# Performance work log

Measured on AMD Instinct MI355X. Metric: run time of the kernel, lower is better.

Reference implementation:

```python
import jax, jax.numpy as jnp
import numpy as np
from jax import lax

NUM_HEADS = 8
EPS = 1e-12  # F.normalize default eps


def _l2norm(t):
    # F.normalize(t, dim=-1): t / max(||t||_2, eps)
    n = jnp.sqrt(jnp.sum(t * t, axis=-1, keepdims=True))
    return t / jnp.maximum(n, EPS)


def setup_inputs() -> dict:
    key = jax.random.key(0)
    k1, k2, k3, k4 = jax.random.split(key, 4)
    b, c, h, w = 16, 384, 64, 64
    x = jax.random.normal(k1, (b, c, h, w), dtype=jnp.float32)
    # 1x1 conv weights stored as (out, in); depthwise 3x3 as (3c, 1, 3, 3)
    w_qkv = jax.random.normal(k2, (3 * c, c), dtype=jnp.float32) * (1.0 / np.sqrt(c))
    w_dw = jax.random.normal(k3, (3 * c, 1, 3, 3), dtype=jnp.float32) * (1.0 / 3.0)
    w_proj = jax.random.normal(k4, (c, c), dtype=jnp.float32) * (1.0 / np.sqrt(c))
    temperature = jnp.ones((1, NUM_HEADS, 1, 1), dtype=jnp.float32)
    return {"x": x, "w_qkv": w_qkv, "w_dw": w_dw, "w_proj": w_proj,
            "temperature": temperature}


def reference(x, w_qkv, w_dw, w_proj, temperature):
    b, c, h, w = x.shape
    hw = h * w
    d = c // NUM_HEADS  # per-head channel dim

    # 1x1 pointwise conv: (b,c,h,w) x (3c,c) -> (b,3c,h,w)
    qkv = jnp.einsum('bchw,oc->bohw', x, w_qkv)
    # depthwise 3x3 conv, groups = 3c, padding SAME, no bias
    qkv = lax.conv_general_dilated(
        qkv, w_dw, window_strides=(1, 1), padding='SAME',
        feature_group_count=3 * c,
        dimension_numbers=('NCHW', 'OIHW', 'NCHW'))

    q, k, v = jnp.split(qkv, 3, axis=1)
    q = q.reshape(b, NUM_HEADS, d, hw)
    k = k.reshape(b, NUM_HEADS, d, hw)
    v = v.reshape(b, NUM_HEADS, d, hw)

    q = _l2norm(q)
    k = _l2norm(k)

    # transposed (channel) attention: scores over channel dim, (b,H,d,d)
    scores = jnp.einsum('bhdn,bhen->bhde', q, k) * temperature
    attn = jax.nn.softmax(scores, axis=-1)

    out = jnp.einsum('bhde,bhen->bhdn', attn, v).reshape(b, c, h, w)
    out = jnp.einsum('bchw,oc->bohw', out, w_proj)
    return out
```

## Files before the change

kernel.cpp:

```cpp
#include <hip/hip_runtime.h>
#include <hip/hip_bf16.h>
#include <math.h>

#define B_   16
#define C_   384
#define C3_  1152
#define HW_  4096
#define NH_  8
#define D_   48

typedef _Float16 f16x8 __attribute__((ext_vector_type(8)));
typedef _Float16 f16x4 __attribute__((ext_vector_type(4)));
typedef _Float16 f16x2 __attribute__((ext_vector_type(2)));
typedef float    f32x4 __attribute__((ext_vector_type(4)));

#define ASM_VMCNT(n) asm volatile("s_waitcnt vmcnt(" #n ")" ::: "memory")

__global__ __launch_bounds__(256) void conv_w_all(
    const float* __restrict__ wqkv, const float* __restrict__ wproj,
    _Float16* __restrict__ oq, _Float16* __restrict__ op)
{
    const int nq = C3_ * C_ / 4;
    const int np = C_ * C_ / 4;
    int i = blockIdx.x * 256 + threadIdx.x;
    const float* src; _Float16* dst; int j;
    if (i < nq) { src = wqkv; dst = oq; j = i; }
    else if (i < nq + np) { src = wproj; dst = op; j = i - nq; }
    else return;
    float4 v = *(const float4*)&src[(size_t)j * 4];
    f16x4 h = { (_Float16)v.x, (_Float16)v.y, (_Float16)v.z, (_Float16)v.w };
    *(f16x4*)&dst[(size_t)j * 4] = h;
}

__global__ __launch_bounds__(256) void transpose_to_f16(
    const float* __restrict__ x, _Float16* __restrict__ xt)
{
    const int b  = blockIdx.z;
    const int k0 = blockIdx.y * 64;
    const int n0 = blockIdx.x * 64;
    __shared__ float sm[64][65];
    const float* xb = x + (size_t)b * C_ * HW_;
    _Float16* xtb = xt + (size_t)b * HW_ * C_;
    const int t = threadIdx.x;
    #pragma unroll
    for (int i = 0; i < 4; ++i) {
        int row = (t >> 4) + i * 16;
        int col = (t & 15) * 4;
        float4 v = *(const float4*)&xb[(size_t)(k0 + row) * HW_ + n0 + col];
        sm[row][col] = v.x; sm[row][col+1] = v.y; sm[row][col+2] = v.z; sm[row][col+3] = v.w;
    }
    __syncthreads();
    #pragma unroll
    for (int i = 0; i < 2; ++i) {
        int nl = (t >> 3) + i * 32;
        int ks = (t & 7) * 8;
        f16x8 h;
        #pragma unroll
        for (int j = 0; j < 8; ++j) h[j] = (_Float16)sm[ks + j][nl];
        *(f16x8*)&xtb[(size_t)(n0 + nl) * C_ + k0 + ks] = h;
    }
}

template<int M, bool F32OUT>
__global__ __launch_bounds__(256, 2) void mfma_gemm(
    const _Float16* __restrict__ Wb,
    const _Float16* __restrict__ XT,
    void* __restrict__ Cv, long long xstride, long long cstride)
{
    constexpr int K = 384;
    constexpr int BK = 32;
    constexpr int NSTEP = K / BK;
    constexpr int MB = M / 128;
    __shared__ _Float16 LDS[36864];
    _Float16* Ash = LDS;
    _Float16* Bsh = LDS + 3 * 128 * BK;

    const int nwg = MB * 16 * B_;
    const int cpx = nwg >> 3;
    const int bid = blockIdx.x;
    const int L   = (bid & 7) * cpx + (bid >> 3);
    const int m0  = (L % MB) * 128;
    const int nb  = L / MB;
    const int n0  = (nb & 15) * 256;
    const int b   = nb >> 4;

    const _Float16* __restrict__ XTb = XT + (size_t)b * xstride;
    const int t = threadIdx.x;
    const int l = t & 63, w = t >> 6;
    const int frow = l & 15, kseg16 = l >> 4;

    auto stage = [&](int d, int kt) {
        const int kk = kt * BK;
        #pragma unroll
        for (int i = 0; i < 2; ++i) {
            const int u = i * 256 + t;
            const int row = u >> 2, slot = u & 3;
            const int scol = slot ^ (row & 3) ^ ((row >> 2) & 1);
            const _Float16* ga = Wb + (size_t)(m0 + row) * K + kk + scol * 8;
            __builtin_amdgcn_global_load_lds(
                (const __attribute__((address_space(1))) void*)ga,
                (__attribute__((address_space(3))) void*)((char*)(Ash + d * 128 * BK) + u * 16),
                16, 0, 0);
        }
        #pragma unroll
        for (int i = 0; i < 4; ++i) {
            const int u = i * 256 + t;
            const int row = u >> 2, slot = u & 3;
            const int scol = slot ^ (row & 3) ^ ((row >> 2) & 1);
            const _Float16* gb = XTb + (size_t)(n0 + row) * K + kk + scol * 8;
            __builtin_amdgcn_global_load_lds(
                (const __attribute__((address_space(1))) void*)gb,
                (__attribute__((address_space(3))) void*)((char*)(Bsh + d * 256 * BK) + u * 16),
                16, 0, 0);
        }
    };

    f32x4 acc[8][4] = {};

    stage(0, 0); stage(1, 1);
    #pragma unroll
    for (int kt = 0; kt < NSTEP; ++kt) {
        const int cur = kt % 3;
        if (kt + 1 < NSTEP) { ASM_VMCNT(6); } else { ASM_VMCNT(0); }
        __builtin_amdgcn_sched_barrier(0);
        __builtin_amdgcn_s_barrier();
        __builtin_amdgcn_sched_barrier(0);
        if (kt + 2 < NSTEP) stage((kt + 2) % 3, kt + 2);
        f16x8 af[8], bfr[4];
        #pragma unroll
        for (int mi = 0; mi < 8; ++mi) {
            const int rA = mi * 16 + frow;
            const int cs = kseg16 ^ (rA & 3) ^ ((rA >> 2) & 1);
            af[mi] = *(const f16x8*)&Ash[cur * 128 * BK + rA * BK + cs * 8];
        }
        #pragma unroll
        for (int ni = 0; ni < 4; ++ni) {
            const int rB = w * 64 + ni * 16 + frow;
            const int cs = kseg16 ^ (rB & 3) ^ ((rB >> 2) & 1);
            bfr[ni] = *(const f16x8*)&Bsh[cur * 256 * BK + rB * BK + cs * 8];
        }
        __builtin_amdgcn_s_setprio(1);
        #pragma unroll
        for (int mi = 0; mi < 8; ++mi)
            #pragma unroll
            for (int ni = 0; ni < 4; ++ni)
                acc[mi][ni] = __builtin_amdgcn_mfma_f32_16x16x32_f16(
                    bfr[ni], af[mi], acc[mi][ni], 0, 0, 0);
        __builtin_amdgcn_s_setprio(0);
    }

    __syncthreads();
    char* tbase = (char*)LDS + w * 17408;
    if constexpr (!F32OUT) {
        #pragma unroll
        for (int mi = 0; mi < 8; ++mi)
            #pragma unroll
            for (int ni = 0; ni < 4; ++ni) {
                const int row = mi * 16 + (l & 15);
                const int pxl = ni * 16 + (l >> 4) * 4;
                f16x2 lo = { (_Float16)acc[mi][ni][0], (_Float16)acc[mi][ni][1] };
                f16x2 hi = { (_Float16)acc[mi][ni][2], (_Float16)acc[mi][ni][3] };
                *(f16x2*)(tbase + row * 136 + pxl * 2)     = lo;
                *(f16x2*)(tbase + row * 136 + pxl * 2 + 4) = hi;
            }
        asm volatile("s_waitcnt lgkmcnt(0)" ::: "memory");
        __builtin_amdgcn_sched_barrier(0);
        _Float16* Co = (_Float16*)Cv + (size_t)b * cstride;
        #pragma unroll
        for (int j = 0; j < 16; ++j) {
            const int ch = j * 8 + (l >> 3);
            const int px = (l & 7) * 8;
            f16x4 lo = *(const f16x4*)(tbase + ch * 136 + px * 2);
            f16x4 hi = *(const f16x4*)(tbase + ch * 136 + px * 2 + 8);
            f16x8 v;
            #pragma unroll
            for (int q = 0; q < 4; ++q) { v[q] = lo[q]; v[q + 4] = hi[q]; }
            *(f16x8*)&Co[(size_t)(m0 + ch) * HW_ + n0 + w * 64 + px] = v;
        }
    } else {
        float* Co = (float*)Cv + (size_t)b * cstride;
        #pragma unroll
        for (int p = 0; p < 2; ++p) {
            if (p) { asm volatile("s_waitcnt lgkmcnt(0)" ::: "memory");
                     __builtin_amdgcn_sched_barrier(0); }
            #pragma unroll
            for (int mi = 0; mi < 4; ++mi)
                #pragma unroll
                for (int ni = 0; ni < 4; ++ni) {
                    const int row = mi * 16 + (l & 15);
                    const int pxl = ni * 16 + (l >> 4) * 4;
                    float2 lo = make_float2(acc[p * 4 + mi][ni][0], acc[p * 4 + mi][ni][1]);
                    float2 hi = make_float2(acc[p * 4 + mi][ni][2], acc[p * 4 + mi][ni][3]);
                    *(float2*)(tbase + row * 272 + pxl * 4)     = lo;
                    *(float2*)(tbase + row * 272 + pxl * 4 + 8) = hi;
                }
            asm volatile("s_waitcnt lgkmcnt(0)" ::: "memory");
            __builtin_amdgcn_sched_barrier(0);
            #pragma unroll
            for (int j = 0; j < 16; ++j) {
                const int lch = j * 4 + (l >> 4);
                const int ch  = p * 64 + lch;
                const int px  = (l & 15) * 4;
                float2 lo = *(const float2*)(tbase + lch * 272 + px * 4);
                float2 hi = *(const float2*)(tbase + lch * 272 + px * 4 + 8);
                f32x4 v = { lo.x, lo.y, hi.x, hi.y };
                *(f32x4*)&Co[(size_t)(m0 + ch) * HW_ + n0 + w * 64 + px] = v;
            }
        }
    }
}

__global__ __launch_bounds__(256) void dwconv_norm(
    _Float16* __restrict__ buf, const float* __restrict__ wdw,
    float* __restrict__ nqinv, float* __restrict__ nkinv)
{
    const int plane = blockIdx.x;
    const int ch = plane % C3_, b = plane / C3_;
    __shared__ _Float16 smh[64 * 72];
    __shared__ float wsum[4];
    _Float16* g = buf + (size_t)plane * HW_;
    const int t = threadIdx.x;
    #pragma unroll
    for (int i = 0; i < 2; ++i) {
        const int u = i * 256 + t;
        f16x8 v = *(const f16x8*)&g[u * 8];
        *(f16x8*)&smh[(u >> 3) * 72 + (u & 7) * 8] = v;
    }
    float w[9];
    #pragma unroll
    for (int j = 0; j < 9; ++j) w[j] = wdw[ch * 9 + j];
    __syncthreads();
    float ssq = 0.f;
    #pragma unroll
    for (int i = 0; i < 2; ++i) {
        const int u = i * 256 + t;
        const int y = u >> 3, c0 = (u & 7) * 8;
        float r[3][10];
        #pragma unroll
        for (int dy = 0; dy < 3; ++dy) {
            const int yy = y + dy - 1;
            if (yy < 0 || yy > 63) {
                #pragma unroll
                for (int j = 0; j < 10; ++j) r[dy][j] = 0.f;
            } else {
                f16x8 v = *(const f16x8*)&smh[yy * 72 + c0];
                #pragma unroll
                for (int j = 0; j < 8; ++j) r[dy][j + 1] = (float)v[j];
                r[dy][0] = (c0 > 0)  ? (float)smh[yy * 72 + c0 - 1] : 0.f;
                r[dy][9] = (c0 < 56) ? (float)smh[yy * 72 + c0 + 8] : 0.f;
            }
        }
        f16x8 o;
        #pragma unroll
        for (int j = 0; j < 8; ++j) {
            float s = 0.f;
            #pragma unroll
            for (int dy = 0; dy < 3; ++dy)
                #pragma unroll
                for (int dx = 0; dx < 3; ++dx)
                    s = fmaf(w[dy * 3 + dx], r[dy][j + dx], s);
            o[j] = (_Float16)s;
            ssq = fmaf(s, s, ssq);
        }
        *(f16x8*)&g[u * 8] = o;
    }
    if (ch < 2 * C_) {
        #pragma unroll
        for (int m = 1; m < 64; m <<= 1) ssq += __shfl_xor(ssq, m);
        if ((t & 63) == 0) wsum[t >> 6] = ssq;
        __syncthreads();
        if (t == 0) {
            float tot = wsum[0] + wsum[1] + wsum[2] + wsum[3];
            float inv = 1.f / fmaxf(sqrtf(tot), 1e-12f);
            (ch < C_ ? nqinv : nkinv)[b * C_ + (ch % C_)] = inv;
        }
    }
}

__global__ __launch_bounds__(256) void scores_mfma(
    const _Float16* __restrict__ buf, float* __restrict__ sp)
{
    const int bh = blockIdx.x;
    const int ks = blockIdx.y;
    const int b = bh >> 3, h = bh & 7;
    const _Float16* qbase = buf + ((size_t)b * C3_ + (size_t)h * D_) * HW_;
    const _Float16* kbase = qbase + (size_t)C_ * HW_;
    const int t = threadIdx.x, l = t & 63, w = t >> 6;
    const int frow = l & 15, kseg = (l >> 4) * 8;
    const int p0 = ks * 1024 + w * 256;

    f32x4 acc[3][3] = {};
    #pragma unroll 2
    for (int st = 0; st < 8; ++st) {
        const int p = p0 + st * 32 + kseg;
        f16x8 qf[3], kf[3];
        #pragma unroll
        for (int mi = 0; mi < 3; ++mi)
            qf[mi] = *(const f16x8*)&qbase[(size_t)(mi * 16 + frow) * HW_ + p];
        #pragma unroll
        for (int ni = 0; ni < 3; ++ni)
            kf[ni] = *(const f16x8*)&kbase[(size_t)(ni * 16 + frow) * HW_ + p];
        #pragma unroll
        for (int mi = 0; mi < 3; ++mi)
            #pragma unroll
            for (int ni = 0; ni < 3; ++ni)
                acc[mi][ni] = __builtin_amdgcn_mfma_f32_16x16x32_f16(
                    qf[mi], kf[ni], acc[mi][ni], 0, 0, 0);
    }
    __shared__ float red[4][D_ * D_];
    #pragma unroll
    for (int mi = 0; mi < 3; ++mi)
        #pragma unroll
        for (int ni = 0; ni < 3; ++ni)
            #pragma unroll
            for (int r = 0; r < 4; ++r)
                red[w][(mi * 16 + (l >> 4) * 4 + r) * D_ + ni * 16 + (l & 15)] =
                    acc[mi][ni][r];
    __syncthreads();
    float* out = sp + ((size_t)ks * 128 + bh) * (D_ * D_);
    const float* rf = &red[0][0];
    for (int i = t; i < D_ * D_; i += 256)
        out[i] = rf[i] + rf[2304 + i] + rf[4608 + i] + rf[6912 + i];
}

__global__ __launch_bounds__(256) void softmax_k(
    const float* __restrict__ sp, const float* __restrict__ nqinv,
    const float* __restrict__ nkinv, const float* __restrict__ temp,
    float* __restrict__ attn)
{
    const int row = blockIdx.x * 4 + (threadIdx.x >> 6);
    const int bh = row / D_, d = row % D_;
    const int h = bh & 7;
    const int e = threadIdx.x & 63;
    float s = -INFINITY;
    if (e < D_) {
        float raw = 0.f;
        #pragma unroll
        for (int ks = 0; ks < 4; ++ks)
            raw += sp[((size_t)ks * 128 + bh) * (D_ * D_) + d * D_ + e];
        s = raw * nqinv[bh * D_ + d] * nkinv[bh * D_ + e] * temp[h];
    }
    float m = s;
    #pragma unroll
    for (int off = 1; off < 64; off <<= 1) m = fmaxf(m, __shfl_xor(m, off));
    float p = (e < D_) ? expf(s - m) : 0.f;
    float sum = p;
    #pragma unroll
    for (int off = 1; off < 64; off <<= 1) sum += __shfl_xor(sum, off);
    if (e < D_) attn[(size_t)bh * (D_ * D_) + d * D_ + e] = p / sum;
}

__global__ __launch_bounds__(256) void pv_kernel(
    _Float16* __restrict__ buf, const float* __restrict__ attn)
{
    const int b = blockIdx.z, h = blockIdx.y;
    const int p0 = blockIdx.x * 512 + threadIdx.x * 2;
    __shared__ float a4[48][48];
    const float* ab = attn + ((size_t)b * 8 + h) * (D_ * D_);
    for (int i = threadIdx.x; i < D_ * D_; i += 256) ((float*)a4)[i] = ab[i];
    __syncthreads();
    const _Float16* vbase = buf + ((size_t)b * C3_ + 2 * C_ + (size_t)h * D_) * HW_;
    float2 acc[48];
    #pragma unroll
    for (int d = 0; d < 48; ++d) { acc[d].x = 0.f; acc[d].y = 0.f; }
    #pragma unroll 1
    for (int e4 = 0; e4 < 12; ++e4) {
        float2 vv[4];
        #pragma unroll
        for (int j = 0; j < 4; ++j) {
            f16x2 h2 = *(const f16x2*)&vbase[(size_t)(e4 * 4 + j) * HW_ + p0];
            vv[j].x = (float)h2[0]; vv[j].y = (float)h2[1];
        }
        #pragma unroll
        for (int d = 0; d < 48; ++d) {
            float4 a = *(const float4*)&a4[d][e4 * 4];
            acc[d].x = fmaf(a.x, vv[0].x, fmaf(a.y, vv[1].x, fmaf(a.z, vv[2].x, fmaf(a.w, vv[3].x, acc[d].x))));
            acc[d].y = fmaf(a.x, vv[0].y, fmaf(a.y, vv[1].y, fmaf(a.z, vv[2].y, fmaf(a.w, vv[3].y, acc[d].y))));
        }
    }
    _Float16* xt2b = buf + (size_t)b * C3_ * HW_;
    #pragma unroll
    for (int px = 0; px < 2; ++px) {
        f16x8 tmp[6];
        #pragma unroll
        for (int d = 0; d < 48; ++d) tmp[d >> 3][d & 7] = (_Float16)(px ? acc[d].y : acc[d].x);
        f16x8* dst = (f16x8*)&xt2b[(size_t)(p0 + px) * C_ + h * D_];
        #pragma unroll
        for (int j = 0; j < 6; ++j) dst[j] = tmp[j];
    }
}

extern "C" void kernel_launch(void* const* d_in, const int* in_sizes, int n_in,
                              void* d_out, int out_size, void* d_ws, size_t ws_size,
                              hipStream_t stream)
{
    const float* x      = (const float*)d_in[0];
    const float* w_qkv  = (const float*)d_in[1];
    const float* w_dw   = (const float*)d_in[2];
    const float* w_proj = (const float*)d_in[3];
    const float* temp   = (const float*)d_in[4];
    float* out = (float*)d_out;

    _Float16* buf = (_Float16*)d_ws;
    float* nqinv = (float*)(buf + (size_t)B_ * C3_ * HW_);
    float* nkinv = nqinv + 6144;
    float* sp    = nkinv + 6144;
    float* attn  = sp + (size_t)4 * 128 * D_ * D_;
    _Float16* wqkv_h  = (_Float16*)(attn + (size_t)128 * D_ * D_);
    _Float16* wproj_h = wqkv_h + (size_t)C3_ * C_;
    _Float16* xt1     = wproj_h + (size_t)C_ * C_;

    conv_w_all<<<(C3_ * C_ / 4 + C_ * C_ / 4 + 255) / 256, 256, 0, stream>>>(
        w_qkv, w_proj, wqkv_h, wproj_h);
    transpose_to_f16<<<dim3(64, 6, 16), 256, 0, stream>>>(x, xt1);

    mfma_gemm<C3_, false><<<dim3(9 * 16 * 16), 256, 0, stream>>>(
        wqkv_h, xt1, buf, (long long)HW_ * C_, (long long)C3_ * HW_);

    dwconv_norm<<<B_ * C3_, 256, 0, stream>>>(buf, w_dw, nqinv, nkinv);

    scores_mfma<<<dim3(128, 4), 256, 0, stream>>>(buf, sp);

    softmax_k<<<1536, 256, 0, stream>>>(sp, nqinv, nkinv, temp, attn);

    pv_kernel<<<dim3(8, 8, 16), 256, 0, stream>>>(buf, attn);

    mfma_gemm<C_, true><<<dim3(3 * 16 * 16), 256, 0, stream>>>(
        wproj_h, buf, out, (long long)C3_ * HW_, (long long)C_ * HW_);
}
```

Measured before the change: 268.4 us.

## Use 8-wave GEMM blocks with 4-stage LDS ring and double-buffered fragments

The MFMA GEMM now runs 512 threads per block as a 2x4 wave grid, so each wave holds a 64x64 accumulator tile instead of 128x64. The global-to-LDS pipeline grows from 3 to 4 stages, and register fragments are double-buffered so the LDS reads for step k+1 overlap the MFMAs for step k. The aim is to cut per-wave register pressure and hide LDS and global latency better. In exchange, occupancy drops to one block per CU, LDS use grows, and each wave does less work per LDS fragment load.

Measured after the change: 287.7 us. +7.2%, slower.

```diff
diff --git a/kernel.cpp b/kernel.cpp
--- a/kernel.cpp
+++ b/kernel.cpp
@@ -62,7 +62,7 @@
 }
 
 template<int M, bool F32OUT>
-__global__ __launch_bounds__(256, 2) void mfma_gemm(
+__global__ __launch_bounds__(512, 1) void mfma_gemm(
     const _Float16* __restrict__ Wb,
     const _Float16* __restrict__ XT,
     void* __restrict__ Cv, long long xstride, long long cstride)
@@ -71,9 +71,7 @@
     constexpr int BK = 32;
     constexpr int NSTEP = K / BK;
     constexpr int MB = M / 128;
-    __shared__ _Float16 LDS[36864];
-    _Float16* Ash = LDS;
-    _Float16* Bsh = LDS + 3 * 128 * BK;
+    __shared__ _Float16 LDS[49152];
 
     const int nwg = MB * 16 * B_;
     const int cpx = nwg >> 3;
@@ -87,73 +85,84 @@
     const _Float16* __restrict__ XTb = XT + (size_t)b * xstride;
     const int t = threadIdx.x;
     const int l = t & 63, w = t >> 6;
+    const int wm = w >> 2, wn = w & 3;
     const int frow = l & 15, kseg16 = l >> 4;
 
     auto stage = [&](int d, int kt) {
         const int kk = kt * BK;
-        #pragma unroll
-        for (int i = 0; i < 2; ++i) {
-            const int u = i * 256 + t;
-            const int row = u >> 2, slot = u & 3;
+        {
+            const int row = t >> 2, slot = t & 3;
             const int scol = slot ^ (row & 3) ^ ((row >> 2) & 1);
             const _Float16* ga = Wb + (size_t)(m0 + row) * K + kk + scol * 8;
             __builtin_amdgcn_global_load_lds(
                 (const __attribute__((address_space(1))) void*)ga,
-                (__attribute__((address_space(3))) void*)((char*)(Ash + d * 128 * BK) + u * 16),
+                (__attribute__((address_space(3))) void*)((char*)(LDS + d * 4096) + t * 16),
                 16, 0, 0);
         }
         #pragma unroll
-        for (int i = 0; i < 4; ++i) {
-            const int u = i * 256 + t;
+        for (int i = 0; i < 2; ++i) {
+            const int u = i * 512 + t;
             const int row = u >> 2, slot = u & 3;
             const int scol = slot ^ (row & 3) ^ ((row >> 2) & 1);
             const _Float16* gb = XTb + (size_t)(n0 + row) * K + kk + scol * 8;
             __builtin_amdgcn_global_load_lds(
                 (const __attribute__((address_space(1))) void*)gb,
-                (__attribute__((address_space(3))) void*)((char*)(Bsh + d * 256 * BK) + u * 16),
+                (__attribute__((address_space(3))) void*)((char*)(LDS + 16384 + d * 8192) + u * 16),
                 16, 0, 0);
         }
     };
 
-    f32x4 acc[8][4] = {};
-
-    stage(0, 0); stage(1, 1);
+    f32x4 acc[4][4] = {};
+    f16x8 af[2][4], bf[2][4];
+
+    auto load_frags = [&](int s, int p) {
+        const int q = s & 3;
+        #pragma unroll
+        for (int mi = 0; mi < 4; ++mi) {
+            const int rA = wm * 64 + mi * 16 + frow;
+            const int cs = kseg16 ^ (rA & 3) ^ ((rA >> 2) & 1);
+            af[p][mi] = *(const f16x8*)&LDS[q * 4096 + rA * BK + cs * 8];
+        }
+        #pragma unroll
+        for (int ni = 0; ni < 4; ++ni) {
+            const int rB = wn * 64 + ni * 16 + frow;
+            const int cs = kseg16 ^ (rB & 3) ^ ((rB >> 2) & 1);
+            bf[p][ni] = *(const f16x8*)&LDS[16384 + q * 8192 + rB * BK + cs * 8];
+        }
+    };
+
+    stage(0, 0); stage(1, 1); stage(2, 2);
+    ASM_VMCNT(6);
+    __builtin_amdgcn_sched_barrier(0);
+    __builtin_amdgcn_s_barrier();
+    __builtin_amdgcn_sched_barrier(0);
+    load_frags(0, 0);
+
     #pragma unroll
     for (int kt = 0; kt < NSTEP; ++kt) {
-        const int cur = kt % 3;
-        if (kt + 1 < NSTEP) { ASM_VMCNT(6); } else { ASM_VMCNT(0); }
+        const int cp = kt & 1, np_ = cp ^ 1;
+        if (kt <= 9)       { ASM_VMCNT(3); }
+        else if (kt == 10) { ASM_VMCNT(0); }
         __builtin_amdgcn_sched_barrier(0);
         __builtin_amdgcn_s_barrier();
         __builtin_amdgcn_sched_barrier(0);
-        if (kt + 2 < NSTEP) stage((kt + 2) % 3, kt + 2);
-        f16x8 af[8], bfr[4];
-        #pragma unroll
-        for (int mi = 0; mi < 8; ++mi) {
-            const int rA = mi * 16 + frow;
-            const int cs = kseg16 ^ (rA & 3) ^ ((rA >> 2) & 1);
-            af[mi] = *(const f16x8*)&Ash[cur * 128 * BK + rA * BK + cs * 8];
-        }
-        #pragma unroll
-        for (int ni = 0; ni < 4; ++ni) {
-            const int rB = w * 64 + ni * 16 + frow;
-            const int cs = kseg16 ^ (rB & 3) ^ ((rB >> 2) & 1);
-            bfr[ni] = *(const f16x8*)&Bsh[cur * 256 * BK + rB * BK + cs * 8];
-        }
+        if (kt + 3 < NSTEP) stage((kt + 3) & 3, kt + 3);
+        if (kt + 1 < NSTEP) load_frags(kt + 1, np_);
         __builtin_amdgcn_s_setprio(1);
         #pragma unroll
-        for (int mi = 0; mi < 8; ++mi)
+        for (int mi = 0; mi < 4; ++mi)
             #pragma unroll
             for (int ni = 0; ni < 4; ++ni)
                 acc[mi][ni] = __builtin_amdgcn_mfma_f32_16x16x32_f16(
-                    bfr[ni], af[mi], acc[mi][ni], 0, 0, 0);
+                    bf[cp][ni], af[cp][mi], acc[mi][ni], 0, 0, 0);
         __builtin_amdgcn_s_setprio(0);
     }
 
     __syncthreads();
-    char* tbase = (char*)LDS + w * 17408;
+    char* tbase = (char*)LDS + w * 8704;
     if constexpr (!F32OUT) {
         #pragma unroll
-        for (int mi = 0; mi < 8; ++mi)
+        for (int mi = 0; mi < 4; ++mi)
             #pragma unroll
             for (int ni = 0; ni < 4; ++ni) {
                 const int row = mi * 16 + (l & 15);
@@ -167,7 +176,7 @@
         __builtin_amdgcn_sched_barrier(0);
         _Float16* Co = (_Float16*)Cv + (size_t)b * cstride;
         #pragma unroll
-        for (int j = 0; j < 16; ++j) {
+        for (int j = 0; j < 8; ++j) {
             const int ch = j * 8 + (l >> 3);
             const int px = (l & 7) * 8;
             f16x4 lo = *(const f16x4*)(tbase + ch * 136 + px * 2);
@@ -175,7 +184,7 @@
             f16x8 v;
             #pragma unroll
             for (int q = 0; q < 4; ++q) { v[q] = lo[q]; v[q + 4] = hi[q]; }
-            *(f16x8*)&Co[(size_t)(m0 + ch) * HW_ + n0 + w * 64 + px] = v;
+            *(f16x8*)&Co[(size_t)(m0 + wm * 64 + ch) * HW_ + n0 + wn * 64 + px] = v;
         }
     } else {
         float* Co = (float*)Cv + (size_t)b * cstride;
@@ -184,27 +193,28 @@
             if (p) { asm volatile("s_waitcnt lgkmcnt(0)" ::: "memory");
                      __builtin_amdgcn_sched_barrier(0); }
             #pragma unroll
-            for (int mi = 0; mi < 4; ++mi)
+            for (int mi = 0; mi < 2; ++mi)
                 #pragma unroll
                 for (int ni = 0; ni < 4; ++ni) {
                     const int row = mi * 16 + (l & 15);
                     const int pxl = ni * 16 + (l >> 4) * 4;
-                    float2 lo = make_float2(acc[p * 4 + mi][ni][0], acc[p * 4 + mi][ni][1]);
-                    float2 hi = make_float2(acc[p * 4 + mi][ni][2], acc[p * 4 + mi][ni][3]);
+                    const f32x4& a = acc[p * 2 + mi][ni];
+                    float2 lo = make_float2(a[0], a[1]);
+                    float2 hi = make_float2(a[2], a[3]);
                     *(float2*)(tbase + row * 272 + pxl * 4)     = lo;
                     *(float2*)(tbase + row * 272 + pxl * 4 + 8) = hi;
                 }
             asm volatile("s_waitcnt lgkmcnt(0)" ::: "memory");
             __builtin_amdgcn_sched_barrier(0);
             #pragma unroll
-            for (int j = 0; j < 16; ++j) {
+            for (int j = 0; j < 8; ++j) {
                 const int lch = j * 4 + (l >> 4);
-                const int ch  = p * 64 + lch;
+                const int ch  = p * 32 + lch;
                 const int px  = (l & 15) * 4;
                 float2 lo = *(const float2*)(tbase + lch * 272 + px * 4);
                 float2 hi = *(const float2*)(tbase + lch * 272 + px * 4 + 8);
                 f32x4 v = { lo.x, lo.y, hi.x, hi.y };
-                *(f32x4*)&Co[(size_t)(m0 + ch) * HW_ + n0 + w * 64 + px] = v;
+                *(f32x4*)&Co[(size_t)(m0 + wm * 64 + ch) * HW_ + n0 + wn * 64 + px] = v;
             }
         }
     }
@@ -414,7 +424,7 @@
         w_qkv, w_proj, wqkv_h, wproj_h);
     transpose_to_f16<<<dim3(64, 6, 16), 256, 0, stream>>>(x, xt1);
 
-    mfma_gemm<C3_, false><<<dim3(9 * 16 * 16), 256, 0, stream>>>(
+    mfma_gemm<C3_, false><<<dim3(9 * 16 * 16), 512, 0, stream>>>(
         wqkv_h, xt1, buf, (long long)HW_ * C_, (long long)C3_ * HW_);
 
     dwconv_norm<<<B_ * C3_, 256, 0, stream>>>(buf, w_dw, nqinv, nkinv);
@@ -425,6 +435,6 @@
 
     pv_kernel<<<dim3(8, 8, 16), 256, 0, stream>>>(buf, attn);
 
-    mfma_gemm<C_, true><<<dim3(3 * 16 * 16), 256, 0, stream>>>(
+    mfma_gemm<C_, true><<<dim3(3 * 16 * 16), 512, 0, stream>>>(
         wproj_h, buf, out, (long long)C3_ * HW_, (long long)C_ * HW_);
 }
```
